# Performance work log

Hardware: AMD Instinct MI355X
Metric: run time of the kernel (lower is better)

The kernel has to match this reference:

```python
import jax, jax.numpy as jnp
import numpy as np

N_NODES = 50000
N_EDGES = 800000
NUM_GRAPHS = 256
D_COUNT = 9
BN_EPS = 1e-5
LRELU_SLOPE = 0.01


def _rbf(d):
    # d: [E]; linspace mu over [0, 6] with 9 centers, sigma = 6/9
    mu = jnp.linspace(0.0, 6.0, D_COUNT)  # [9]
    sigma = 6.0 / D_COUNT
    return jnp.exp(-(((d[:, None] - mu[None, :]) / sigma) ** 2))  # [E, 9]


def _interaction_layer(x, pos, row, col, Wc, bc, Wn, bn, g, be):
    # per-edge gather of positions, RBF radial embedding
    coord_diff = pos[row] - pos[col]                       # [E, 3]
    d = jnp.linalg.norm(coord_diff, axis=-1)               # [E]
    radial = jax.nn.silu(_rbf(d) @ Wc + bc)                # [E, C]
    # message = x_j * radial; scatter-add to target nodes (col)
    msg = x[row] * radial                                  # [E, C]
    agg = jax.ops.segment_sum(msg, col, num_segments=x.shape[0])  # [N, C]
    # mlp_node_cov: Linear -> Dropout(eval: identity) -> LeakyReLU -> BatchNorm1d(eval, fresh stats)
    h = (x + agg) @ Wn + bn
    h = jnp.where(h > 0, h, LRELU_SLOPE * h)
    h = g * h / jnp.sqrt(jnp.asarray(1.0 + BN_EPS, h.dtype)) + be
    return h


def setup_inputs() -> dict:
    key = jax.random.key(0)
    ks = jax.random.split(key, 16)
    C_IN, C_H = 64, 128
    inp = {
        "x": jax.random.normal(ks[0], (N_NODES, C_IN), jnp.float32),
        "pos": jax.random.normal(ks[1], (N_NODES, 3), jnp.float32) * 3.0,
        "edge_index": jax.random.randint(ks[2], (2, N_EDGES), 0, N_NODES, jnp.int32),
        "batch": jnp.sort(jax.random.randint(ks[3], (N_NODES,), 0, NUM_GRAPHS, jnp.int32)),
        "W_lin": jax.random.normal(ks[4], (C_IN, C_H), jnp.float32) / np.sqrt(C_IN),
        "b_lin": jnp.zeros((C_H,), jnp.float32),
    }
    for i, l in enumerate(("1", "2", "3")):
        kk = jax.random.split(ks[5 + i], 2)
        inp["Wc" + l] = jax.random.normal(kk[0], (D_COUNT, C_H), jnp.float32) / np.sqrt(D_COUNT)
        inp["bc" + l] = jnp.zeros((C_H,), jnp.float32)
        inp["Wn" + l] = jax.random.normal(kk[1], (C_H, C_H), jnp.float32) / np.sqrt(C_H)
        inp["bn" + l] = jnp.zeros((C_H,), jnp.float32)
        inp["g" + l] = jnp.ones((C_H,), jnp.float32)
        inp["be" + l] = jnp.zeros((C_H,), jnp.float32)
    return inp


def reference(x, pos, edge_index, batch, W_lin, b_lin,
              Wc1, bc1, Wn1, bn1, g1, be1,
              Wc2, bc2, Wn2, bn2, g2, be2,
              Wc3, bc3, Wn3, bn3, g3, be3):
    row, col = edge_index[0], edge_index[1]
    h = jax.nn.silu(x @ W_lin + b_lin)
    h = _interaction_layer(h, pos, row, col, Wc1, bc1, Wn1, bn1, g1, be1)
    h = _interaction_layer(h, pos, row, col, Wc2, bc2, Wn2, bn2, g2, be2)
    h = _interaction_layer(h, pos, row, col, Wc3, bc3, Wn3, bn3, g3, be3)
    # global_add_pool
    return jax.ops.segment_sum(h, batch, num_segments=NUM_GRAPHS)
```

## Files before the change

kernel.cpp:

```cpp
#include <hip/hip_runtime.h>
#include <hip/hip_fp16.h>
#include <math.h>

#define N_NODES 50000
#define N_EDGES 800000
#define NUM_GRAPHS 256
#define C_IN 64
#define C_H 128
#define D_COUNT 9
#define LRELU_SLOPE 0.01f
#define TAB_BINS 8192
#define TAB_SCALE 1024.0f
#define WEDGES 64
#define NCHUNK (N_EDGES / WEDGES)
#define NBUCK ((N_NODES + 255) / 256)
#define REGION_CAP 6144
#define SCAT_BLK_EDGES 2048
#define TBLK (TAB_BINS * 64 / 256)
#define WNBLK 8
#define ZBLK 1024
#define LIN0BLK ((N_NODES + 31) / 32)
#define OUTZBLK 32
#define OFF1 (3 * TBLK)
#define OFF2 (OFF1 + 3 * WNBLK)
#define OFF3 (OFF2 + ZBLK)
#define OFF4 (OFF3 + LIN0BLK)
#define OFF5 (OFF4 + OUTZBLK)
#define SETUP_GRID (OFF5 + 1)

typedef _Float16 half8_t __attribute__((ext_vector_type(8)));
typedef float f32x4_t __attribute__((ext_vector_type(4)));

__device__ __forceinline__ float fast_rcp(float x) { return __builtin_amdgcn_rcpf(x); }
__device__ __forceinline__ __half2 u2h2(unsigned int u) { return __builtin_bit_cast(__half2, u); }
__device__ __forceinline__ unsigned int h22u(__half2 h) { return __builtin_bit_cast(unsigned int, h); }

__device__ __forceinline__ void atomic_pk_add_h2(unsigned int* addr, unsigned int val) {
    asm volatile("global_atomic_pk_add_f16 %0, %1, off"
                 :: "v"(addr), "v"(val) : "memory");
}

__global__ __launch_bounds__(256) void setup_kernel(
        const float* __restrict__ Wc1, const float* __restrict__ bc1,
        const float* __restrict__ Wc2, const float* __restrict__ bc2,
        const float* __restrict__ Wc3, const float* __restrict__ bc3,
        const float* __restrict__ Wn1, const float* __restrict__ Wn2,
        const float* __restrict__ Wn3,
        const float* __restrict__ x, const float* __restrict__ Wl,
        const float* __restrict__ bl,
        unsigned int* __restrict__ tabh, unsigned int* __restrict__ Wnh,
        uint4* __restrict__ aggz, unsigned int* __restrict__ hhf,
        uint4* __restrict__ outz, int* __restrict__ bcur) {
    __shared__ float xs[32][C_IN];
    const int b = blockIdx.x;
    const int t = threadIdx.x;
    if (b < OFF1) {
        const int l = b / TBLK;
        const float* Wc = (l == 0) ? Wc1 : (l == 1) ? Wc2 : Wc3;
        const float* bc = (l == 0) ? bc1 : (l == 1) ? bc2 : bc3;
        const int idx = (b - l * TBLK) * 256 + t;
        const int lane = idx & 63;
        const int bin = idx >> 6;
        const float d = ((float)bin + 0.5f) * (1.0f / TAB_SCALE);
        float v[2];
#pragma unroll
        for (int p = 0; p < 2; ++p) {
            const int c = 2 * lane + p;
            float a = bc[c];
#pragma unroll
            for (int k = 0; k < D_COUNT; ++k) {
                const float u = (d - 0.75f * (float)k) * 1.5f;
                a = fmaf(__expf(-u * u), Wc[k * C_H + c], a);
            }
            v[p] = a * fast_rcp(1.0f + __expf(-a));
        }
        tabh[(size_t)l * TAB_BINS * 64 + idx] = h22u(__floats2half2_rn(v[0], v[1]));
    } else if (b < OFF2) {
        const int bb = b - OFF1;
        const int l = bb / WNBLK;
        const float* Wn = (l == 0) ? Wn1 : (l == 1) ? Wn2 : Wn3;
        const int idx = (bb - l * WNBLK) * 256 + t;
        const int lane = idx & 63;
        const int tile = idx >> 6;
        const int kc = tile >> 3, ct = tile & 7;
        const int q = lane >> 4, r = lane & 15;
        half8_t v;
#pragma unroll
        for (int j = 0; j < 8; ++j)
            v[j] = (_Float16)Wn[(size_t)(kc * 32 + 8 * q + j) * C_H + ct * 16 + r];
        ((uint4*)Wnh)[(size_t)l * 2048 + idx] = __builtin_bit_cast(uint4, v);
    } else if (b < OFF3) {
        const int n16 = N_NODES * 16;
        const int stride = ZBLK * 256;
        for (int i = (b - OFF2) * 256 + t; i < n16; i += stride)
            aggz[i] = make_uint4(0u, 0u, 0u, 0u);
    } else if (b < OFF4) {
        const int node0 = (b - OFF3) * 32;
        for (int i = t * 4; i < 32 * C_IN; i += 256 * 4) {
            const int n = i >> 6;
            const int c = i & 63;
            if (node0 + n < N_NODES)
                *(float4*)&xs[n][c] = *(const float4*)&x[(size_t)(node0 + n) * C_IN + c];
        }
        __syncthreads();
        const int wv = t >> 6;
        const int lane = t & 63;
        const int nb = wv * 8;
        const float2 b2 = *(const float2*)&bl[2 * lane];
        float2 acc[8];
#pragma unroll
        for (int n = 0; n < 8; ++n) acc[n] = b2;
        for (int k = 0; k < C_IN; k += 4) {
            const float2 w0 = *(const float2*)&Wl[(size_t)(k + 0) * C_H + 2 * lane];
            const float2 w1 = *(const float2*)&Wl[(size_t)(k + 1) * C_H + 2 * lane];
            const float2 w2 = *(const float2*)&Wl[(size_t)(k + 2) * C_H + 2 * lane];
            const float2 w3 = *(const float2*)&Wl[(size_t)(k + 3) * C_H + 2 * lane];
#pragma unroll
            for (int n = 0; n < 8; ++n) {
                const float4 sv = *(const float4*)&xs[nb + n][k];
                acc[n].x = fmaf(sv.x, w0.x, acc[n].x); acc[n].y = fmaf(sv.x, w0.y, acc[n].y);
                acc[n].x = fmaf(sv.y, w1.x, acc[n].x); acc[n].y = fmaf(sv.y, w1.y, acc[n].y);
                acc[n].x = fmaf(sv.z, w2.x, acc[n].x); acc[n].y = fmaf(sv.z, w2.y, acc[n].y);
                acc[n].x = fmaf(sv.w, w3.x, acc[n].x); acc[n].y = fmaf(sv.w, w3.y, acc[n].y);
            }
        }
#pragma unroll
        for (int n = 0; n < 8; ++n) {
            const int node = node0 + nb + n;
            if (node < N_NODES) {
                const float ax = acc[n].x, ay = acc[n].y;
                const float sx = ax * fast_rcp(1.0f + __expf(-ax));
                const float sy = ay * fast_rcp(1.0f + __expf(-ay));
                hhf[(size_t)node * 64 + lane] = h22u(__floats2half2_rn(sx, sy));
            }
        }
    } else if (b < OFF5) {
        const int n16 = NUM_GRAPHS * C_H / 4;
        const int stride = OUTZBLK * 256;
        for (int i = (b - OFF4) * 256 + t; i < n16; i += stride)
            outz[i] = make_uint4(0u, 0u, 0u, 0u);
    } else {
        if (t < NBUCK) bcur[t] = 0;
    }
}

__global__ __launch_bounds__(256) void bscatter_kernel(
        const int* __restrict__ row, const int* __restrict__ col,
        const float* __restrict__ pos, int* __restrict__ bcur, uint2* __restrict__ ebuf) {
    __shared__ int lhist[NBUCK];
    __shared__ int lcur[NBUCK];
    const int t = threadIdx.x;
    const int e0 = blockIdx.x * SCAT_BLK_EDGES;
    for (int i = t; i < NBUCK; i += 256) lhist[i] = 0;
    __syncthreads();

    int myb[8];
    uint2 myrec[8];
#pragma unroll
    for (int s = 0; s < 8; ++s) {
        const int e = e0 + s * 256 + t;
        if (e < N_EDGES) {
            const int r = row[e];
            const int c = col[e];
            const float dx = pos[r * 3 + 0] - pos[c * 3 + 0];
            const float dy = pos[r * 3 + 1] - pos[c * 3 + 1];
            const float dz = pos[r * 3 + 2] - pos[c * 3 + 2];
            const float d = sqrtf(dx * dx + dy * dy + dz * dz);
            int bin = (int)(d * TAB_SCALE);
            bin = bin < TAB_BINS - 1 ? bin : TAB_BINS - 1;
            myb[s] = c >> 8;
            myrec[s] = make_uint2((unsigned int)r | ((unsigned int)c << 16),
                                  (unsigned int)bin);
            atomicAdd(&lhist[myb[s]], 1);
        } else {
            myb[s] = -1;
        }
    }
    __syncthreads();
    for (int i = t; i < NBUCK; i += 256)
        lcur[i] = (lhist[i] > 0) ? atomicAdd(&bcur[i], lhist[i]) : 0;
    __syncthreads();
#pragma unroll
    for (int s = 0; s < 8; ++s) {
        if (myb[s] >= 0) {
            const int p = atomicAdd(&lcur[myb[s]], 1);
            ebuf[(size_t)myb[s] * REGION_CAP + p] = myrec[s];
        }
    }
}

__global__ __launch_bounds__(256) void bsort_kernel(
        const uint2* __restrict__ ebuf, const int* __restrict__ bcur,
        uint2* __restrict__ rcb) {
    __shared__ uint2 se[REGION_CAP];
    __shared__ int lhist[256];
    __shared__ int lcur[256];
    __shared__ int csc[256];
    const int b = blockIdx.x;
    const int t = threadIdx.x;
    csc[t] = (t < NBUCK) ? bcur[t] : 0;
    __syncthreads();
    for (int d = 1; d < 256; d <<= 1) {
        const int x = (t >= d) ? csc[t - d] : 0;
        __syncthreads();
        csc[t] += x;
        __syncthreads();
    }
    const int dbase = (b == 0) ? 0 : csc[b - 1];
    const int n = bcur[b];

    const uint2* src = ebuf + (size_t)b * REGION_CAP;
    for (int i = t; i < n; i += 256) se[i] = src[i];
    lhist[t] = 0;
    __syncthreads();
    for (int i = t; i < n; i += 256)
        atomicAdd(&lhist[(se[i].x >> 16) & 255u], 1);
    __syncthreads();
    int v = lhist[t];
    int sv = v;
    lcur[t] = v;
    __syncthreads();
    for (int d = 1; d < 256; d <<= 1) {
        const int x = (t >= d) ? lcur[t - d] : 0;
        __syncthreads();
        lcur[t] += x;
        __syncthreads();
        sv = lcur[t];
    }
    __syncthreads();
    lcur[t] = sv - v;
    __syncthreads();
    for (int i = t; i < n; i += 256) {
        const uint2 e = se[i];
        const int dst = atomicAdd(&lcur[(e.x >> 16) & 255u], 1);
        rcb[dbase + dst] = e;
    }
}

__global__ __launch_bounds__(256) void aggregate_kernel(
        const unsigned int* __restrict__ hhf, const uint2* __restrict__ rcb,
        const unsigned int* __restrict__ tabh, unsigned int* __restrict__ aggh) {
    __shared__ uint2 meta[4][WEDGES];
    const int t = threadIdx.x;
    const int lane = t & 63;
    const int wv = t >> 6;
    const int base = (blockIdx.x * 4 + wv) * WEDGES;

    const __half2 hzero = __floats2half2_rn(0.0f, 0.0f);

    meta[wv][lane] = rcb[base + lane];
    asm volatile("s_waitcnt lgkmcnt(0)" ::: "memory");
    __builtin_amdgcn_sched_barrier(0);
    __builtin_amdgcn_wave_barrier();

    unsigned int huA[8], huB[8], huC[8];
    unsigned int tvA[8], tvB[8], tvC[8];
    int colA[8], colB[8], colC[8];
    __half2 acc2 = hzero;
    float2 accf = make_float2(0.0f, 0.0f);
    int sCur;
    bool first = true;

#define LOADG(g, HU, TV, CO)                                                  \
    {                                                                         \
        _Pragma("unroll")                                                     \
        for (int u = 0; u < 8; ++u) {                                         \
            const uint2 m = meta[wv][(g) * 8 + u];                            \
            const unsigned int rcu = __builtin_amdgcn_readfirstlane(m.x);     \
            const int sBin = __builtin_amdgcn_readfirstlane((int)m.y);        \
            const int sRow = (int)(rcu & 0xffffu);                            \
            CO[u] = (int)(rcu >> 16);                                         \
            HU[u] = hhf[(size_t)sRow * 64 + lane];                            \
            TV[u] = tabh[(size_t)sBin * 64 + lane];                           \
        }                                                                     \
    }

#define COMPUTEG(HU, TV, CO)                                                  \
    {                                                                         \
        _Pragma("unroll")                                                     \
        for (int u = 0; u < 8; ++u) {                                         \
            if (CO[u] != sCur) {                                              \
                const float2 pf = __half22float2(acc2);                       \
                accf.x += pf.x; accf.y += pf.y; acc2 = hzero;                 \
                unsigned int* dst = &aggh[(size_t)sCur * 64 + lane];          \
                const unsigned int hv = h22u(__floats2half2_rn(accf.x, accf.y)); \
                if (first) {                                                  \
                    atomic_pk_add_h2(dst, hv);                                \
                    first = false;                                            \
                } else {                                                      \
                    *dst = hv;                                                \
                }                                                             \
                accf.x = 0.0f; accf.y = 0.0f;                                 \
                sCur = CO[u];                                                 \
            }                                                                 \
            acc2 = __hfma2(u2h2(HU[u]), u2h2(TV[u]), acc2);                   \
        }                                                                     \
        const float2 pg = __half22float2(acc2);                               \
        accf.x += pg.x; accf.y += pg.y; acc2 = hzero;                         \
    }

    LOADG(0, huA, tvA, colA);
    LOADG(1, huB, tvB, colB);
    LOADG(2, huC, tvC, colC);
    sCur = colA[0];
    COMPUTEG(huA, tvA, colA);
    LOADG(3, huA, tvA, colA);
    COMPUTEG(huB, tvB, colB);
    LOADG(4, huB, tvB, colB);
    COMPUTEG(huC, tvC, colC);
    LOADG(5, huC, tvC, colC);
    COMPUTEG(huA, tvA, colA);
    LOADG(6, huA, tvA, colA);
    COMPUTEG(huB, tvB, colB);
    LOADG(7, huB, tvB, colB);
    COMPUTEG(huC, tvC, colC);
    COMPUTEG(huA, tvA, colA);
    COMPUTEG(huB, tvB, colB);

    {
        unsigned int* dst = &aggh[(size_t)sCur * 64 + lane];
        atomic_pk_add_h2(dst, h22u(__floats2half2_rn(accf.x, accf.y)));
    }
#undef LOADG
#undef COMPUTEG
}

template <int POOL, int ZERO>
__global__ __launch_bounds__(256) void node_kernel(
        unsigned int* __restrict__ hhf, unsigned int* __restrict__ aggh,
        const uint4* __restrict__ Wnb, const float* __restrict__ bn,
        const float* __restrict__ g, const float* __restrict__ be,
        const int* __restrict__ batch, float* __restrict__ out) {
    __shared__ unsigned short sA[32 * 136];
    const int node0 = blockIdx.x * 32;
    const int t = threadIdx.x;
    for (int i = t; i < 32 * 64; i += 256) {
        const int n = i >> 6;
        const int p = i & 63;
        if (node0 + n < N_NODES) {
            const unsigned int hv = hhf[(size_t)(node0 + n) * 64 + p];
            const unsigned int av = aggh[(size_t)(node0 + n) * 64 + p];
            if (ZERO) aggh[(size_t)(node0 + n) * 64 + p] = 0u;
            *(unsigned int*)&sA[n * 136 + 2 * p] = h22u(__hadd2(u2h2(hv), u2h2(av)));
        } else {
            *(unsigned int*)&sA[n * 136 + 2 * p] = 0u;
        }
    }
    __syncthreads();
    const int lane = t & 63;
    const int wv = t >> 6;
    const int q = lane >> 4;
    const int r = lane & 15;
    const int ct0 = 2 * wv, ct1 = 2 * wv + 1;
    const int c0 = ct0 * 16 + r, c1 = ct1 * 16 + r;
    const float bn0 = bn[c0], bn1 = bn[c1];
    f32x4_t acc00 = {bn0, bn0, bn0, bn0};
    f32x4_t acc01 = {bn1, bn1, bn1, bn1};
    f32x4_t acc10 = {bn0, bn0, bn0, bn0};
    f32x4_t acc11 = {bn1, bn1, bn1, bn1};
#pragma unroll
    for (int kc = 0; kc < 4; ++kc) {
        const half8_t a0 = __builtin_bit_cast(half8_t,
            *(const uint4*)&sA[(size_t)r * 136 + kc * 32 + 8 * q]);
        const half8_t a1 = __builtin_bit_cast(half8_t,
            *(const uint4*)&sA[(size_t)(16 + r) * 136 + kc * 32 + 8 * q]);
        const half8_t b0 = __builtin_bit_cast(half8_t, Wnb[(kc * 8 + ct0) * 64 + lane]);
        const half8_t b1 = __builtin_bit_cast(half8_t, Wnb[(kc * 8 + ct1) * 64 + lane]);
        acc00 = __builtin_amdgcn_mfma_f32_16x16x32_f16(a0, b0, acc00, 0, 0, 0);
        acc01 = __builtin_amdgcn_mfma_f32_16x16x32_f16(a0, b1, acc01, 0, 0, 0);
        acc10 = __builtin_amdgcn_mfma_f32_16x16x32_f16(a1, b0, acc10, 0, 0, 0);
        acc11 = __builtin_amdgcn_mfma_f32_16x16x32_f16(a1, b1, acc11, 0, 0, 0);
    }
    const float inv = 0.9999950000374997f;
    const float gv0 = g[c0] * inv, gv1 = g[c1] * inv;
    const float be0 = be[c0], be1 = be[c1];
    if (POOL == 0) {
        unsigned short* hp = (unsigned short*)hhf;
#pragma unroll
        for (int rt = 0; rt < 2; ++rt) {
            const f32x4_t aA = rt ? acc10 : acc00;
            const f32x4_t aB = rt ? acc11 : acc01;
#pragma unroll
            for (int i = 0; i < 4; ++i) {
                const int node = node0 + rt * 16 + 4 * q + i;
                if (node < N_NODES) {
                    float v0 = aA[i]; v0 = v0 > 0.0f ? v0 : LRELU_SLOPE * v0;
                    float v1 = aB[i]; v1 = v1 > 0.0f ? v1 : LRELU_SLOPE * v1;
                    hp[(size_t)node * C_H + c0] =
                        __builtin_bit_cast(unsigned short, (_Float16)fmaf(gv0, v0, be0));
                    hp[(size_t)node * C_H + c1] =
                        __builtin_bit_cast(unsigned short, (_Float16)fmaf(gv1, v1, be1));
                }
            }
        }
    } else {
        float pacc0 = 0.0f, pacc1 = 0.0f;
        int curb = -1;
#pragma unroll
        for (int rt = 0; rt < 2; ++rt) {
            const f32x4_t aA = rt ? acc10 : acc00;
            const f32x4_t aB = rt ? acc11 : acc01;
#pragma unroll
            for (int i = 0; i < 4; ++i) {
                const int node = node0 + rt * 16 + 4 * q + i;
                if (node < N_NODES) {
                    float v0 = aA[i]; v0 = v0 > 0.0f ? v0 : LRELU_SLOPE * v0;
                    float v1 = aB[i]; v1 = v1 > 0.0f ? v1 : LRELU_SLOPE * v1;
                    const float o0 = fmaf(gv0, v0, be0);
                    const float o1 = fmaf(gv1, v1, be1);
                    const int bb = batch[node];
                    if (bb != curb) {
                        if (curb >= 0) {
                            atomicAdd(&out[curb * C_H + c0], pacc0);
                            atomicAdd(&out[curb * C_H + c1], pacc1);
                        }
                        pacc0 = 0.0f; pacc1 = 0.0f;
                        curb = bb;
                    }
                    pacc0 += o0;
                    pacc1 += o1;
                }
            }
        }
        if (curb >= 0) {
            atomicAdd(&out[curb * C_H + c0], pacc0);
            atomicAdd(&out[curb * C_H + c1], pacc1);
        }
    }
}

extern "C" void kernel_launch(void* const* d_in, const int* in_sizes, int n_in,
                              void* d_out, int out_size, void* d_ws, size_t ws_size,
                              hipStream_t stream) {
    const float* x     = (const float*)d_in[0];
    const float* pos   = (const float*)d_in[1];
    const int*   eidx  = (const int*)d_in[2];
    const int*   batch = (const int*)d_in[3];
    const float* W_lin = (const float*)d_in[4];
    const float* b_lin = (const float*)d_in[5];

    unsigned int* aggh = (unsigned int*)d_ws;
    unsigned int* hhf  = aggh + (size_t)N_NODES * 64;
    unsigned int* Wnh  = hhf + (size_t)N_NODES * 64;
    unsigned int* tabh = Wnh + 3 * C_H * 64;
    int* bcur = (int*)(tabh + 3 * (size_t)TAB_BINS * 64);
    uintptr_t p = (uintptr_t)(bcur + NBUCK);
    p = (p + 15) & ~(uintptr_t)15;
    uint2* ebuf = (uint2*)p;
    uint2* rcb  = ebuf + (size_t)NBUCK * REGION_CAP;

    const int* row = eidx;
    const int* col = eidx + N_EDGES;

    hipLaunchKernelGGL(setup_kernel, dim3(SETUP_GRID), dim3(256), 0, stream,
                       (const float*)d_in[6],  (const float*)d_in[7],
                       (const float*)d_in[12], (const float*)d_in[13],
                       (const float*)d_in[18], (const float*)d_in[19],
                       (const float*)d_in[8],  (const float*)d_in[14],
                       (const float*)d_in[20],
                       x, W_lin, b_lin,
                       tabh, Wnh, (uint4*)aggh, hhf, (uint4*)d_out, bcur);

    hipLaunchKernelGGL(bscatter_kernel,
                       dim3((N_EDGES + SCAT_BLK_EDGES - 1) / SCAT_BLK_EDGES), dim3(256),
                       0, stream, row, col, pos, bcur, ebuf);
    hipLaunchKernelGGL(bsort_kernel, dim3(NBUCK), dim3(256), 0, stream,
                       ebuf, bcur, rcb);

    for (int l = 0; l < 3; ++l) {
        const float* bn = (const float*)d_in[6 + l * 6 + 3];
        const float* g  = (const float*)d_in[6 + l * 6 + 4];
        const float* be = (const float*)d_in[6 + l * 6 + 5];
        unsigned int* tab_l = tabh + (size_t)l * TAB_BINS * 64;
        const uint4* Wnb_l = (const uint4*)Wnh + (size_t)l * 2048;

        hipLaunchKernelGGL(aggregate_kernel, dim3(NCHUNK / 4), dim3(256), 0, stream,
                           hhf, rcb, tab_l, aggh);
        if (l < 2) {
            hipLaunchKernelGGL(HIP_KERNEL_NAME(node_kernel<0, 1>),
                               dim3((N_NODES + 31) / 32), dim3(256), 0, stream,
                               hhf, aggh, Wnb_l, bn, g, be, batch, (float*)d_out);
        } else {
            hipLaunchKernelGGL(HIP_KERNEL_NAME(node_kernel<1, 0>),
                               dim3((N_NODES + 31) / 32), dim3(256), 0, stream,
                               hhf, aggh, Wnb_l, bn, g, be, batch, (float*)d_out);
        }
    }
}
```

Measured before the change: 211.7 us.

## Remap aggregate blocks per XCD, deepen edge prefetch, vectorize node loads

The aggregate kernel now remaps block IDs so that each of the eight XCDs handles a contiguous range of edge chunks. This should improve L2 locality for the sorted edges and their target rows. It also drops the shared-memory staging of edge metadata in favour of direct wave-uniform global loads, and deepens the software prefetch from three to four groups of eight edges, which raises register pressure. The node kernel now loads h and agg and zeroes agg with 128-bit vector accesses instead of 32-bit ones, cutting the number of memory instructions.

After: 211.2 us. About the same (-0.2%).

```diff
diff --git a/kernel.cpp b/kernel.cpp
--- a/kernel.cpp
+++ b/kernel.cpp
@@ -13,6 +13,7 @@
 #define TAB_SCALE 1024.0f
 #define WEDGES 64
 #define NCHUNK (N_EDGES / WEDGES)
+#define NAGG (NCHUNK / 4)
 #define NBUCK ((N_NODES + 255) / 256)
 #define REGION_CAP 6144
 #define SCAT_BLK_EDGES 2048
@@ -240,22 +241,20 @@
 __global__ __launch_bounds__(256) void aggregate_kernel(
         const unsigned int* __restrict__ hhf, const uint2* __restrict__ rcb,
         const unsigned int* __restrict__ tabh, unsigned int* __restrict__ aggh) {
-    __shared__ uint2 meta[4][WEDGES];
+    const int bid = blockIdx.x;
+    const int xcd = bid & 7, ix = bid >> 3;
+    const int qq = NAGG >> 3, rr = NAGG & 7;
+    const int blk = (xcd < rr ? xcd * (qq + 1) : rr * (qq + 1) + (xcd - rr) * qq) + ix;
     const int t = threadIdx.x;
     const int lane = t & 63;
-    const int wv = t >> 6;
-    const int base = (blockIdx.x * 4 + wv) * WEDGES;
+    const int wv = __builtin_amdgcn_readfirstlane(t >> 6);
+    const size_t base = (size_t)(blk * 4 + wv) * WEDGES;
 
     const __half2 hzero = __floats2half2_rn(0.0f, 0.0f);
 
-    meta[wv][lane] = rcb[base + lane];
-    asm volatile("s_waitcnt lgkmcnt(0)" ::: "memory");
-    __builtin_amdgcn_sched_barrier(0);
-    __builtin_amdgcn_wave_barrier();
-
-    unsigned int huA[8], huB[8], huC[8];
-    unsigned int tvA[8], tvB[8], tvC[8];
-    int colA[8], colB[8], colC[8];
+    unsigned int huA[8], huB[8], huC[8], huD[8];
+    unsigned int tvA[8], tvB[8], tvC[8], tvD[8];
+    int colA[8], colB[8], colC[8], colD[8];
     __half2 acc2 = hzero;
     float2 accf = make_float2(0.0f, 0.0f);
     int sCur;
@@ -265,7 +264,7 @@
     {                                                                         \
         _Pragma("unroll")                                                     \
         for (int u = 0; u < 8; ++u) {                                         \
-            const uint2 m = meta[wv][(g) * 8 + u];                            \
+            const uint2 m = rcb[base + (g) * 8 + u];                          \
             const unsigned int rcu = __builtin_amdgcn_readfirstlane(m.x);     \
             const int sBin = __builtin_amdgcn_readfirstlane((int)m.y);        \
             const int sRow = (int)(rcu & 0xffffu);                            \
@@ -302,20 +301,20 @@
     LOADG(0, huA, tvA, colA);
     LOADG(1, huB, tvB, colB);
     LOADG(2, huC, tvC, colC);
+    LOADG(3, huD, tvD, colD);
     sCur = colA[0];
     COMPUTEG(huA, tvA, colA);
-    LOADG(3, huA, tvA, colA);
+    LOADG(4, huA, tvA, colA);
     COMPUTEG(huB, tvB, colB);
-    LOADG(4, huB, tvB, colB);
+    LOADG(5, huB, tvB, colB);
     COMPUTEG(huC, tvC, colC);
-    LOADG(5, huC, tvC, colC);
-    COMPUTEG(huA, tvA, colA);
-    LOADG(6, huA, tvA, colA);
-    COMPUTEG(huB, tvB, colB);
-    LOADG(7, huB, tvB, colB);
-    COMPUTEG(huC, tvC, colC);
+    LOADG(6, huC, tvC, colC);
+    COMPUTEG(huD, tvD, colD);
+    LOADG(7, huD, tvD, colD);
     COMPUTEG(huA, tvA, colA);
     COMPUTEG(huB, tvB, colB);
+    COMPUTEG(huC, tvC, colC);
+    COMPUTEG(huD, tvD, colD);
 
     {
         unsigned int* dst = &aggh[(size_t)sCur * 64 + lane];
@@ -334,17 +333,27 @@
     __shared__ unsigned short sA[32 * 136];
     const int node0 = blockIdx.x * 32;
     const int t = threadIdx.x;
-    for (int i = t; i < 32 * 64; i += 256) {
-        const int n = i >> 6;
-        const int p = i & 63;
-        if (node0 + n < N_NODES) {
-            const unsigned int hv = hhf[(size_t)(node0 + n) * 64 + p];
-            const unsigned int av = aggh[(size_t)(node0 + n) * 64 + p];
-            if (ZERO) aggh[(size_t)(node0 + n) * 64 + p] = 0u;
-            *(unsigned int*)&sA[n * 136 + 2 * p] = h22u(__hadd2(u2h2(hv), u2h2(av)));
+    const uint4* hh4 = (const uint4*)hhf;
+    uint4* ag4 = (uint4*)aggh;
+    for (int i = t; i < 32 * 16; i += 256) {
+        const int n = i >> 4;
+        const int pp = i & 15;
+        const int node = node0 + n;
+        uint4 hv, av;
+        if (node < N_NODES) {
+            hv = hh4[(size_t)node * 16 + pp];
+            av = ag4[(size_t)node * 16 + pp];
+            if (ZERO) ag4[(size_t)node * 16 + pp] = make_uint4(0u, 0u, 0u, 0u);
         } else {
-            *(unsigned int*)&sA[n * 136 + 2 * p] = 0u;
-        }
+            hv = make_uint4(0u, 0u, 0u, 0u);
+            av = hv;
+        }
+        uint4 sv;
+        sv.x = h22u(__hadd2(u2h2(hv.x), u2h2(av.x)));
+        sv.y = h22u(__hadd2(u2h2(hv.y), u2h2(av.y)));
+        sv.z = h22u(__hadd2(u2h2(hv.z), u2h2(av.z)));
+        sv.w = h22u(__hadd2(u2h2(hv.w), u2h2(av.w)));
+        *(uint4*)&sA[n * 136 + 8 * pp] = sv;
     }
     __syncthreads();
     const int lane = t & 63;
@@ -474,7 +483,7 @@
         unsigned int* tab_l = tabh + (size_t)l * TAB_BINS * 64;
         const uint4* Wnb_l = (const uint4*)Wnh + (size_t)l * 2048;
 
-        hipLaunchKernelGGL(aggregate_kernel, dim3(NCHUNK / 4), dim3(256), 0, stream,
+        hipLaunchKernelGGL(aggregate_kernel, dim3(NAGG), dim3(256), 0, stream,
                            hhf, rcb, tab_l, aggh);
         if (l < 2) {
             hipLaunchKernelGGL(HIP_KERNEL_NAME(node_kernel<0, 1>),
```
